# Optimization experiments

Hardware: AMD Instinct MI355X
Metric: run time of the kernel (lower is better)

The kernel has to match this reference:

```python
import jax, jax.numpy as jnp
import numpy as np

GATE_DECAY = 3.0

def setup_inputs() -> dict:
    key = jax.random.key(0)
    ks = jax.random.split(key, 4)
    B, S, D, I = 8, 2048, 512, 2048
    x = jax.random.normal(ks[0], (B, S, D), dtype=jnp.float32)
    # kaiming normal fan_in, linear gain: std = 1/sqrt(fan_in)
    Wa = jax.random.normal(ks[1], (I, D), dtype=jnp.float32) / np.sqrt(D)
    Wi = jax.random.normal(ks[2], (I, D), dtype=jnp.float32) / np.sqrt(D)
    ba = jnp.zeros((I,), dtype=jnp.float32)
    bi = jnp.zeros((I,), dtype=jnp.float32)
    lo, hi = np.log(0.9 / 0.1), np.log(0.999 / 0.001)  # logit(0.9), logit(0.999)
    gate = jax.random.uniform(ks[3], (I,), dtype=jnp.float32, minval=lo, maxval=hi)
    return {"x": x, "Wa": Wa, "ba": ba, "Wi": Wi, "bi": bi, "gate": gate}

def reference(x, Wa, ba, Wi, bi, gate):
    # Precompute both projections for all timesteps as large GEMMs.
    pa = jnp.einsum('bsd,id->bsi', x, Wa) + ba   # [B,S,I]
    pi = jnp.einsum('bsd,id->bsi', x, Wi) + bi   # [B,S,I]
    reset_gate = jax.nn.sigmoid(pa)
    input_gate = jax.nn.sigmoid(pi)
    alpha = jax.nn.sigmoid(gate)                  # [I]
    adaptive_alpha = alpha / (GATE_DECAY ** reset_gate)          # [B,S,I]
    drive = jnp.sqrt(1.0 - adaptive_alpha ** 2) * (input_gate * pi)
    B, S, I = pa.shape

    def step(h, ac):
        a, c = ac
        h = a * h + c
        return h, h

    h0 = jnp.zeros((B, I), dtype=x.dtype)
    # scan over time: move S to leading axis
    _, ys = jax.lax.scan(step, h0, (adaptive_alpha.transpose(1, 0, 2), drive.transpose(1, 0, 2)))
    return ys.transpose(1, 0, 2)  # [B,S,I]
```

## Files before the change

kernel.cpp:

```cpp
#include <hip/hip_runtime.h>


#define LOG2_3 1.5849625007211562f

typedef _Float16 f16x8 __attribute__((ext_vector_type(8)));
typedef _Float16 f16x4 __attribute__((ext_vector_type(4)));
typedef _Float16 f16x2 __attribute__((ext_vector_type(2)));
typedef float f32x4 __attribute__((ext_vector_type(4)));

__device__ __forceinline__ float sigmoid_fast(float v) {
  return __fdividef(1.0f, 1.0f + __expf(-v));
}

__device__ __forceinline__ void async_copy16(void* lds, const void* gp) {
  __builtin_amdgcn_global_load_lds((__attribute__((address_space(1))) void*)gp,
                                   (__attribute__((address_space(3))) void*)lds,
                                   16, 0, 0);
}

__global__ __launch_bounds__(256) void cvt_all(const float* __restrict__ x,
                                               const float* __restrict__ Wa,
                                               const float* __restrict__ Wi,
                                               _Float16* __restrict__ xh,
                                               _Float16* __restrict__ wh) {
  int idx = blockIdx.x * 256 + threadIdx.x;
  const float* src;
  _Float16* dst;
  int off, doff;
  if (idx < 2097152) {
    src = x; dst = xh; off = idx; doff = idx;
  } else if (idx < 2097152 + 262144) {
    src = Wa; dst = wh; off = idx - 2097152;
    doff = off + ((off >> 7) << 7);
  } else {
    src = Wi; dst = wh; off = idx - 2359296;
    doff = off + ((off >> 7) << 7) + 128;
  }
  float4 v = ((const float4*)src)[off];
  f16x4 h;
  h[0] = (_Float16)v.x;
  h[1] = (_Float16)v.y;
  h[2] = (_Float16)v.z;
  h[3] = (_Float16)v.w;
  ((f16x4*)dst)[doff] = h;
}

__device__ __forceinline__ void gate_ac(float pa, float pi, float alpha, float& a, float& c) {
  float rg = sigmoid_fast(pa);
  a = alpha * exp2f(-LOG2_3 * rg);
  float ig = sigmoid_fast(pi);
  float m = fmaxf(1.0f - a * a, 1e-8f);
  c = (m * __frsqrt_rn(m)) * (ig * pi);
}

__global__ __launch_bounds__(512) void gemm_gate(const _Float16* __restrict__ Ah,
                                                 const _Float16* __restrict__ Wh,
                                                 const float* __restrict__ ba,
                                                 const float* __restrict__ bi,
                                                 const float* __restrict__ gate,
                                                 _Float16* __restrict__ AC,
                                                 float2* __restrict__ agg) {
  constexpr int K = 512;
  constexpr int N2 = 4096;
  __shared__ __align__(16) _Float16 smem[32768];
  const int t = threadIdx.x;
  const int bx = blockIdx.x;
  const int by = blockIdx.y;
  const int mBase = by * 256;
  const int nBase = bx * 256;
  const int r = t >> 2;
  const int p = t & 3;
  const int lsw = p ^ ((r >> 1) & 3);
  const _Float16* gA0 = Ah + (size_t)(mBase + r) * K + lsw * 8;
  const _Float16* gB0 = Wh + (size_t)(nBase + r) * K + lsw * 8;
  const int ldst = r * 32 + p * 8;

  const int lane = t & 63;
  const int wave = t >> 6;
  const int wm = (wave & 1) * 128;
  const int wn = (wave >> 1) * 64;
  const int lrow = lane & 15;
  const int quad = lane >> 4;
  const int xq = quad ^ ((lrow >> 1) & 3);

  f32x4 acc[8][4];
#pragma unroll
  for (int i = 0; i < 8; ++i)
#pragma unroll
    for (int j = 0; j < 4; ++j)
      acc[i][j] = (f32x4)0.0f;

  _Float16* b0 = smem;
  _Float16* b1 = smem + 16384;

  auto STAGE = [&](int tt, _Float16* bb) {
    const int ko = tt * 32;
    async_copy16(bb + ldst, gA0 + ko);
    async_copy16(bb + 4096 + ldst, gA0 + (size_t)128 * K + ko);
    async_copy16(bb + 8192 + ldst, gB0 + ko);
    async_copy16(bb + 12288 + ldst, gB0 + (size_t)128 * K + ko);
  };

  STAGE(0, b0);
  __syncthreads();

#pragma unroll
  for (int kt = 0; kt < 16; ++kt) {
    _Float16* cur = (kt & 1) ? b1 : b0;
    _Float16* nxt = (kt & 1) ? b0 : b1;
    if (kt < 15) STAGE(kt + 1, nxt);
    f16x8 af[8], bf[4];
#pragma unroll
    for (int i = 0; i < 8; ++i)
      af[i] = *(const f16x8*)(cur + (wm + i * 16 + lrow) * 32 + xq * 8);
#pragma unroll
    for (int j = 0; j < 4; ++j)
      bf[j] = *(const f16x8*)(cur + 8192 + (wn + j * 16 + lrow) * 32 + xq * 8);
#pragma unroll
    for (int i = 0; i < 8; ++i)
#pragma unroll
      for (int j = 0; j < 4; ++j)
        acc[i][j] = __builtin_amdgcn_mfma_f32_16x16x32_f16(af[i], bf[j], acc[i][j], 0, 0, 0);
    __syncthreads();
  }

  float bias[4];
#pragma unroll
  for (int j = 0; j < 4; ++j) {
    const int n = nBase + wn + j * 16 + lrow;
    bias[j] = (n & 1) ? bi[n >> 1] : ba[n >> 1];
  }

  _Float16* cst = smem;
  float* pAs = (float*)(smem + 18432);
  float* pHs = pAs + 16 * 132;

  const int col = t & 127;
  const int q = t >> 7;
  const float alpha = sigmoid_fast(gate[(nBase >> 1) + col]);
  const int b = by >> 3;

#pragma unroll
  for (int h = 0; h < 4; ++h) {
    if (wm == (h >> 1) * 128) {
      const int i0f = (h & 1) * 4;
#pragma unroll
      for (int ii = 0; ii < 4; ++ii)
#pragma unroll
        for (int j = 0; j < 4; ++j)
#pragma unroll
          for (int rr = 0; rr < 4; ++rr)
            cst[(ii * 16 + quad * 4 + rr) * 264 + wn + j * 16 + lrow] =
                (_Float16)(acc[i0f + ii][j][rr] + bias[j]);
    }
    __syncthreads();
    float A = 1.0f, Hn = 0.0f;
    _Float16* ACp = AC + (size_t)(mBase + h * 64 + q * 16) * N2 + nBase + 2 * col;
#pragma unroll 4
    for (int rs = 0; rs < 16; ++rs) {
      f16x2 pp = *(const f16x2*)(cst + (q * 16 + rs) * 264 + 2 * col);
      float a, c;
      gate_ac((float)pp[0], (float)pp[1], alpha, a, c);
      f16x2 o;
      o[0] = (_Float16)a;
      o[1] = (_Float16)c;
      *(f16x2*)ACp = o;
      ACp += N2;
      A *= a;
      Hn = fmaf(a, Hn, c);
    }
    pAs[(h * 4 + q) * 132 + col] = A;
    pHs[(h * 4 + q) * 132 + col] = Hn;
    __syncthreads();
  }

  if (t < 128) {
#pragma unroll
    for (int k = 0; k < 8; ++k) {
      float A0 = pAs[(2 * k) * 132 + t], H0 = pHs[(2 * k) * 132 + t];
      float A1 = pAs[(2 * k + 1) * 132 + t], H1 = pHs[(2 * k + 1) * 132 + t];
      const int ch = ((by & 7) << 3) + k;
      agg[((size_t)(b * 64 + ch)) * 2048 + (nBase >> 1) + t] =
          make_float2(A0 * A1, fmaf(A1, H0, H1));
    }
  }
}

__global__ __launch_bounds__(64) void scan_pass2(const float2* __restrict__ agg,
                                                 float* __restrict__ carry) {
  const int i = blockIdx.x * 64 + threadIdx.x;
  const int b = blockIdx.y;
  float h = 0.0f;
  for (int c8 = 0; c8 < 8; ++c8) {
    float2 aH[8];
#pragma unroll
    for (int u = 0; u < 8; ++u)
      aH[u] = agg[((size_t)(b * 64 + c8 * 8 + u)) * 2048 + i];
#pragma unroll
    for (int u = 0; u < 8; ++u) {
      carry[((size_t)(b * 64 + c8 * 8 + u)) * 2048 + i] = h;
      h = fmaf(aH[u].x, h, aH[u].y);
    }
  }
}

__global__ __launch_bounds__(256) void scan_out(const _Float16* __restrict__ AC,
                                                const float* __restrict__ carry,
                                                float* __restrict__ out) {
  const int tt = blockIdx.x * 256 + threadIdx.x;
  const int i0 = tt * 4;
  const int ch = blockIdx.y;
  const int b = blockIdx.z;
  const float4 cr = ((const float4*)(carry + ((size_t)(b * 64 + ch)) * 2048))[tt];
  float h0 = cr.x, h1 = cr.y, h2 = cr.z, h3 = cr.w;
  const _Float16* row = AC + ((size_t)(b * 2048 + ch * 32)) * 4096 + i0 * 2;
  float* orow = out + ((size_t)(b * 2048 + ch * 32)) * 2048 + i0;

  f16x8 va[4], vb[4];
#pragma unroll
  for (int u = 0; u < 4; ++u)
    va[u] = __builtin_nontemporal_load((const f16x8*)(row + (size_t)u * 4096));

#pragma unroll
  for (int p = 0; p < 8; ++p) {
    if (p < 7) {
      const _Float16* nrow = row + (size_t)(p + 1) * 4 * 4096;
      f16x8* dst = (p & 1) ? va : vb;
#pragma unroll
      for (int u = 0; u < 4; ++u)
        dst[u] = __builtin_nontemporal_load((const f16x8*)(nrow + (size_t)u * 4096));
    }
    const f16x8* v = (p & 1) ? vb : va;
    float* op = orow + (size_t)p * 4 * 2048;
#pragma unroll
    for (int u = 0; u < 4; ++u) {
      h0 = fmaf((float)v[u][0], h0, (float)v[u][1]);
      h1 = fmaf((float)v[u][2], h1, (float)v[u][3]);
      h2 = fmaf((float)v[u][4], h2, (float)v[u][5]);
      h3 = fmaf((float)v[u][6], h3, (float)v[u][7]);
      f32x4 o;
      o[0] = h0;
      o[1] = h1;
      o[2] = h2;
      o[3] = h3;
      __builtin_nontemporal_store(o, (f32x4*)(op + (size_t)u * 2048));
    }
  }
}

extern "C" void kernel_launch(void* const* d_in, const int* in_sizes, int n_in,
                              void* d_out, int out_size, void* d_ws, size_t ws_size,
                              hipStream_t stream) {
  const float* x = (const float*)d_in[0];
  const float* Wa = (const float*)d_in[1];
  const float* ba = (const float*)d_in[2];
  const float* Wi = (const float*)d_in[3];
  const float* bi = (const float*)d_in[4];
  const float* gate = (const float*)d_in[5];
  float* out = (float*)d_out;

  char* ws = (char*)d_ws;
  _Float16* xh = (_Float16*)ws;
  _Float16* wh = (_Float16*)(ws + 16777216);
  const size_t MN2 = (size_t)16384 * 4096;
  _Float16* AC = (_Float16*)(ws + 20971520);
  float2* agg = (float2*)(ws + 20971520 + MN2 * 2);
  float* carry = (float*)(ws + 20971520 + MN2 * 2 + 8388608);

  cvt_all<<<10240, 256, 0, stream>>>(x, Wa, Wi, xh, wh);
  gemm_gate<<<dim3(16, 64), 512, 0, stream>>>(xh, wh, ba, bi, gate, AC, agg);
  scan_pass2<<<dim3(32, 8), 64, 0, stream>>>(agg, carry);
  scan_out<<<dim3(2, 64, 8), 256, 0, stream>>>(AC, carry, out);
}
```

Measured before the change: 331.4 us.

## Split gate math out of GEMM epilogue, store raw projections in fragment layout

The GEMM now writes its biased fp16 projections straight from MFMA accumulator registers in a fragment-native layout, dropping the LDS staging and in-epilogue gate computation. A new gate_agg kernel reads those projections to compute per-chunk scan aggregates, and scan_out recomputes the gate nonlinearities on the fly instead of reading precomputed a/c. This shortens the GEMM epilogue and its syncs, but adds one extra full read of the projection buffer and duplicates the transcendental work. scan_out now stores scalar floats per thread rather than float4 vectors.

```diff
diff --git a/kernel.cpp b/kernel.cpp
--- a/kernel.cpp
+++ b/kernel.cpp
@@ -53,15 +53,12 @@
   c = (m * __frsqrt_rn(m)) * (ig * pi);
 }
 
-__global__ __launch_bounds__(512) void gemm_gate(const _Float16* __restrict__ Ah,
-                                                 const _Float16* __restrict__ Wh,
-                                                 const float* __restrict__ ba,
-                                                 const float* __restrict__ bi,
-                                                 const float* __restrict__ gate,
-                                                 _Float16* __restrict__ AC,
-                                                 float2* __restrict__ agg) {
+__global__ __launch_bounds__(512) void gemm_pp(const _Float16* __restrict__ Ah,
+                                               const _Float16* __restrict__ Wh,
+                                               const float* __restrict__ ba,
+                                               const float* __restrict__ bi,
+                                               _Float16* __restrict__ PP) {
   constexpr int K = 512;
-  constexpr int N2 = 4096;
   __shared__ __align__(16) _Float16 smem[32768];
   const int t = threadIdx.x;
   const int bx = blockIdx.x;
@@ -131,59 +128,54 @@
     bias[j] = (n & 1) ? bi[n >> 1] : ba[n >> 1];
   }
 
-  _Float16* cst = smem;
-  float* pAs = (float*)(smem + 18432);
-  float* pHs = pAs + 16 * 132;
-
-  const int col = t & 127;
-  const int q = t >> 7;
-  const float alpha = sigmoid_fast(gate[(nBase >> 1) + col]);
-  const int b = by >> 3;
-
-#pragma unroll
-  for (int h = 0; h < 4; ++h) {
-    if (wm == (h >> 1) * 128) {
-      const int i0f = (h & 1) * 4;
-#pragma unroll
-      for (int ii = 0; ii < 4; ++ii)
-#pragma unroll
-        for (int j = 0; j < 4; ++j)
-#pragma unroll
-          for (int rr = 0; rr < 4; ++rr)
-            cst[(ii * 16 + quad * 4 + rr) * 264 + wn + j * 16 + lrow] =
-                (_Float16)(acc[i0f + ii][j][rr] + bias[j]);
-    }
-    __syncthreads();
-    float A = 1.0f, Hn = 0.0f;
-    _Float16* ACp = AC + (size_t)(mBase + h * 64 + q * 16) * N2 + nBase + 2 * col;
-#pragma unroll 4
-    for (int rs = 0; rs < 16; ++rs) {
-      f16x2 pp = *(const f16x2*)(cst + (q * 16 + rs) * 264 + 2 * col);
+  _Float16* pp = PP + (((size_t)by * 16 + bx) << 16) + wave * 8192 + lane * 4;
+#pragma unroll
+  for (int i = 0; i < 8; ++i)
+#pragma unroll
+    for (int j = 0; j < 4; ++j) {
+      f16x4 v;
+#pragma unroll
+      for (int rr = 0; rr < 4; ++rr)
+        v[rr] = (_Float16)(acc[i][j][rr] + bias[j]);
+      *(f16x4*)(pp + i * 1024 + j * 256) = v;
+    }
+}
+
+__global__ __launch_bounds__(256) void gate_agg(const _Float16* __restrict__ PP,
+                                                const float* __restrict__ gate,
+                                                float2* __restrict__ agg) {
+  const int tt = blockIdx.x * 256 + threadIdx.x;
+  const int ch = blockIdx.y;
+  const int b = blockIdx.z;
+  const float alpha = sigmoid_fast(gate[tt]);
+  const int n = tt * 2;
+  const int bx = n >> 8;
+  const int nl = n & 255;
+  const int wn_idx = nl >> 6;
+  const int j = (nl >> 4) & 3;
+  const int lrow = nl & 15;
+  const int by = b * 8 + (ch >> 3);
+  const int c8 = ch & 7;
+  const int wm_bit = c8 >> 2;
+  const _Float16* base = PP + (((size_t)by * 16 + bx) << 16) +
+                         (wm_bit + 2 * wn_idx) * 8192 + j * 256 + lrow * 4;
+  f16x8 v[8];
+#pragma unroll
+  for (int u = 0; u < 8; ++u) {
+    const int i = (c8 * 2 + (u >> 2)) & 7;
+    v[u] = *(const f16x8*)(base + i * 1024 + (u & 3) * 64);
+  }
+  float A = 1.0f, H = 0.0f;
+#pragma unroll
+  for (int u = 0; u < 8; ++u)
+#pragma unroll
+    for (int rr = 0; rr < 4; ++rr) {
       float a, c;
-      gate_ac((float)pp[0], (float)pp[1], alpha, a, c);
-      f16x2 o;
-      o[0] = (_Float16)a;
-      o[1] = (_Float16)c;
-      *(f16x2*)ACp = o;
-      ACp += N2;
+      gate_ac((float)v[u][rr], (float)v[u][4 + rr], alpha, a, c);
       A *= a;
-      Hn = fmaf(a, Hn, c);
-    }
-    pAs[(h * 4 + q) * 132 + col] = A;
-    pHs[(h * 4 + q) * 132 + col] = Hn;
-    __syncthreads();
-  }
-
-  if (t < 128) {
-#pragma unroll
-    for (int k = 0; k < 8; ++k) {
-      float A0 = pAs[(2 * k) * 132 + t], H0 = pHs[(2 * k) * 132 + t];
-      float A1 = pAs[(2 * k + 1) * 132 + t], H1 = pHs[(2 * k + 1) * 132 + t];
-      const int ch = ((by & 7) << 3) + k;
-      agg[((size_t)(b * 64 + ch)) * 2048 + (nBase >> 1) + t] =
-          make_float2(A0 * A1, fmaf(A1, H0, H1));
-    }
-  }
+      H = fmaf(a, H, c);
+    }
+  agg[((size_t)(b * 64 + ch)) * 2048 + tt] = make_float2(A, H);
 }
 
 __global__ __launch_bounds__(64) void scan_pass2(const float2* __restrict__ agg,
@@ -204,48 +196,43 @@
   }
 }
 
-__global__ __launch_bounds__(256) void scan_out(const _Float16* __restrict__ AC,
+__global__ __launch_bounds__(256) void scan_out(const _Float16* __restrict__ PP,
+                                                const float* __restrict__ gate,
                                                 const float* __restrict__ carry,
                                                 float* __restrict__ out) {
   const int tt = blockIdx.x * 256 + threadIdx.x;
-  const int i0 = tt * 4;
   const int ch = blockIdx.y;
   const int b = blockIdx.z;
-  const float4 cr = ((const float4*)(carry + ((size_t)(b * 64 + ch)) * 2048))[tt];
-  float h0 = cr.x, h1 = cr.y, h2 = cr.z, h3 = cr.w;
-  const _Float16* row = AC + ((size_t)(b * 2048 + ch * 32)) * 4096 + i0 * 2;
-  float* orow = out + ((size_t)(b * 2048 + ch * 32)) * 2048 + i0;
-
-  f16x8 va[4], vb[4];
-#pragma unroll
-  for (int u = 0; u < 4; ++u)
-    va[u] = __builtin_nontemporal_load((const f16x8*)(row + (size_t)u * 4096));
-
-#pragma unroll
-  for (int p = 0; p < 8; ++p) {
-    if (p < 7) {
-      const _Float16* nrow = row + (size_t)(p + 1) * 4 * 4096;
-      f16x8* dst = (p & 1) ? va : vb;
-#pragma unroll
-      for (int u = 0; u < 4; ++u)
-        dst[u] = __builtin_nontemporal_load((const f16x8*)(nrow + (size_t)u * 4096));
-    }
-    const f16x8* v = (p & 1) ? vb : va;
-    float* op = orow + (size_t)p * 4 * 2048;
-#pragma unroll
-    for (int u = 0; u < 4; ++u) {
-      h0 = fmaf((float)v[u][0], h0, (float)v[u][1]);
-      h1 = fmaf((float)v[u][2], h1, (float)v[u][3]);
-      h2 = fmaf((float)v[u][4], h2, (float)v[u][5]);
-      h3 = fmaf((float)v[u][6], h3, (float)v[u][7]);
-      f32x4 o;
-      o[0] = h0;
-      o[1] = h1;
-      o[2] = h2;
-      o[3] = h3;
-      __builtin_nontemporal_store(o, (f32x4*)(op + (size_t)u * 2048));
-    }
-  }
+  const float alpha = sigmoid_fast(gate[tt]);
+  float h = carry[((size_t)(b * 64 + ch)) * 2048 + tt];
+  const int n = tt * 2;
+  const int bx = n >> 8;
+  const int nl = n & 255;
+  const int wn_idx = nl >> 6;
+  const int j = (nl >> 4) & 3;
+  const int lrow = nl & 15;
+  const int by = b * 8 + (ch >> 3);
+  const int c8 = ch & 7;
+  const int wm_bit = c8 >> 2;
+  const _Float16* base = PP + (((size_t)by * 16 + bx) << 16) +
+                         (wm_bit + 2 * wn_idx) * 8192 + j * 256 + lrow * 4;
+  f16x8 v[8];
+#pragma unroll
+  for (int u = 0; u < 8; ++u) {
+    const int i = (c8 * 2 + (u >> 2)) & 7;
+    v[u] = *(const f16x8*)(base + i * 1024 + (u & 3) * 64);
+  }
+  float* orow = out + ((size_t)(b * 2048 + ch * 32)) * 2048 + tt;
+#pragma unroll
+  for (int u = 0; u < 8; ++u)
+#pragma unroll
+    for (int rr = 0; rr < 4; ++rr) {
+      float a, c;
+      gate_ac((float)v[u][rr], (float)v[u][4 + rr], alpha, a, c);
+      h = fmaf(a, h, c);
+      __builtin_nontemporal_store(h, orow);
+      orow += 2048;
+    }
 }
 
 extern "C" void kernel_launch(void* const* d_in, const int* in_sizes, int n_in,
@@ -263,12 +250,13 @@
   _Float16* xh = (_Float16*)ws;
   _Float16* wh = (_Float16*)(ws + 16777216);
   const size_t MN2 = (size_t)16384 * 4096;
-  _Float16* AC = (_Float16*)(ws + 20971520);
+  _Float16* PP = (_Float16*)(ws + 20971520);
   float2* agg = (float2*)(ws + 20971520 + MN2 * 2);
   float* carry = (float*)(ws + 20971520 + MN2 * 2 + 8388608);
 
   cvt_all<<<10240, 256, 0, stream>>>(x, Wa, Wi, xh, wh);
-  gemm_gate<<<dim3(16, 64), 512, 0, stream>>>(xh, wh, ba, bi, gate, AC, agg);
+  gemm_pp<<<dim3(16, 64), 512, 0, stream>>>(xh, wh, ba, bi, PP);
+  gate_agg<<<dim3(8, 64, 8), 256, 0, stream>>>(PP, gate, agg);
   scan_pass2<<<dim3(32, 8), 64, 0, stream>>>(agg, carry);
-  scan_out<<<dim3(2, 64, 8), 256, 0, stream>>>(AC, carry, out);
-}
+  scan_out<<<dim3(8, 64, 8), 256, 0, stream>>>(PP, gate, carry, out);
+}
```

Measured after the change: 333.0 us. Within noise of the previous version (+0.5%).
